# Optimization experiments

Measured on AMD Instinct MI355X. Metric: run time of the kernel, lower is better.

The kernel has to match this reference:

```python
import jax, jax.numpy as jnp
import numpy as np

RADIUS = 0.1
K = 32
NUM_GROUPS = 8
EPS = 1e-5
B, N = 2, 4096
IN_DIM = 13
OUT_DIMS = (64, 64, 128)


def _safe_norm(x, axis=-1, keepdims=False):
    # 2-norm with zero (not NaN) gradient at 0; forward identical to jnp.linalg.norm
    sq = jnp.sum(x * x, axis=axis, keepdims=keepdims)
    nz = sq > 0
    return jnp.where(nz, jnp.sqrt(jnp.where(nz, sq, 1.0)), 0.0)


def _angle(v1, v2):
    y = _safe_norm(jnp.cross(v1, v2), axis=-1)
    x = jnp.sum(v1 * v2, axis=-1)
    deg = (y == 0) & (x == 0)  # degenerate pairs (e.g. self-neighbor): atan2(0,0)=0
    return jnp.where(deg, 0.0, jnp.arctan2(y, jnp.where(deg, 1.0, x)))


def _ball_group(xyz, radius, k):
    # xyz: (B,N,3) -> neighbor indices (B,N,K); pad out-of-radius slots with first valid idx
    b, n, _ = xyz.shape
    sq = jnp.sum((xyz[:, :, None, :] - xyz[:, None, :, :]) ** 2, axis=-1)  # (B,N,N)
    idx = jnp.broadcast_to(jnp.arange(n, dtype=jnp.int32), (b, n, n))
    idx = jnp.where(sq > radius * radius, n, idx)
    idx = jnp.sort(idx, axis=-1)[:, :, :k]  # (B,N,K)
    first = idx[:, :, :1]
    return jnp.where(idx == n, first, idx)


def _group_norm(x, gamma, beta):
    # x: (B,C,K,N), torch GroupNorm(8, C) semantics (biased var, eps=1e-5)
    b, c, k, n = x.shape
    xg = x.reshape(b, NUM_GROUPS, c // NUM_GROUPS, k, n)
    m = jnp.mean(xg, axis=(2, 3, 4), keepdims=True)
    v = jnp.var(xg, axis=(2, 3, 4), keepdims=True)
    xn = ((xg - m) * jax.lax.rsqrt(v + EPS)).reshape(b, c, k, n)
    return xn * gamma[None, :, None, None] + beta[None, :, None, None]


def _forward(feature, xyz, conv0_w, gn0_g, gn0_b, conv1_w, gn1_g, gn1_b,
             conv2_w, gn2_g, gn2_b, wa, wb, wc):
    b = xyz.shape[0]
    idx = _ball_group(xyz, RADIUS, K)                     # (B,N,K) int32
    bidx = jnp.arange(b)[:, None, None]
    grouped_xyz = xyz[bidx, idx]                          # (B,N,K,3)
    grouped_xyz1 = grouped_xyz - xyz[:, :, None, :]       # relative coords
    dists = _safe_norm(grouped_xyz1, axis=-1, keepdims=True)
    grouped_n = feature[bidx, idx]                        # grouped normals (B,N,K,3)
    new_points = jnp.concatenate([grouped_xyz1, dists, grouped_n], axis=-1)  # (B,N,K,7)

    nr = feature[:, :, None, :]                           # (B,N,1,3)
    ppf = jnp.stack([_angle(nr, grouped_xyz1),
                     _angle(grouped_n, grouped_xyz1),
                     _angle(nr, grouped_n)], axis=-1)     # (B,N,K,3)

    xyz6 = jnp.concatenate([jnp.broadcast_to(xyz[:, :, None, :], grouped_xyz.shape),
                            grouped_xyz], axis=-1)        # (B,N,K,6)
    fused = jnp.concatenate([wa * xyz6, wb * new_points[..., :4], wc * ppf], axis=-1)  # (B,N,K,13)

    x = jnp.transpose(fused, (0, 3, 2, 1))                # (B,13,K,N)
    layers = [(conv0_w, gn0_g, gn0_b), (conv1_w, gn1_g, gn1_b), (conv2_w, gn2_g, gn2_b)]
    for i, (w, g, bb) in enumerate(layers):
        x = jnp.einsum('oc,bckn->bokn', w, x)             # 1x1 conv, no bias
        x = _group_norm(x, g, bb)
        if i != len(layers) - 1:
            x = jax.nn.relu(x)
    out = jnp.max(jax.nn.relu(x), axis=2)                 # (B,128,N)
    x = jnp.max(x, axis=2)                                # (B,128,N)
    return (out, x)


def setup_inputs() -> dict:
    key = jax.random.key(0)
    ks = jax.random.split(key, 8)
    xyz = jax.random.uniform(ks[0], (B, N, 3), dtype=jnp.float32)
    feature = jax.random.normal(ks[1], (B, N, 3), dtype=jnp.float32)
    feature = feature / _safe_norm(feature, axis=-1, keepdims=True)  # unit normals
    inp = {'feature': feature, 'xyz': xyz}
    dims = [IN_DIM] + list(OUT_DIMS)
    for i in range(3):
        scale = 1.0 / np.sqrt(dims[i])
        inp[f'conv{i}_w'] = (jax.random.normal(ks[2 + i], (dims[i + 1], dims[i]), dtype=jnp.float32) * scale)
        inp[f'gn{i}_g'] = jnp.ones((dims[i + 1],), jnp.float32)
        inp[f'gn{i}_b'] = jnp.zeros((dims[i + 1],), jnp.float32)
    inp['wa'] = jnp.ones((1,), jnp.float32)
    inp['wb'] = jnp.ones((1,), jnp.float32)
    inp['wc'] = jnp.ones((1,), jnp.float32)
    return inp


def reference(feature, xyz, conv0_w, gn0_g, gn0_b, conv1_w, gn1_g, gn1_b,
              conv2_w, gn2_g, gn2_b, wa, wb, wc):
    return _forward(feature, xyz, conv0_w, gn0_g, gn0_b, conv1_w, gn1_g, gn1_b,
                    conv2_w, gn2_g, gn2_b, wa, wb, wc)
```

## Files before the change

kernel.cpp:

```cpp
#include <hip/hip_runtime.h>
#include <hip/hip_bf16.h>

#define DEVINL __device__ __forceinline__

typedef short short8 __attribute__((ext_vector_type(8)));
typedef float f32x4 __attribute__((ext_vector_type(4)));

namespace {
constexpr int NB = 2;
constexpr int NN = 4096;
constexpr int KK = 32;
constexpr int NP = NN * KK;
constexpr float R2 = 0.01f;
constexpr float GEPS = 1e-5f;
}

DEVINL ushort2 splitbf(float v) {
    unsigned int b = __float_as_uint(v);
    unsigned int hb = b & 0xffff0000u;
    float r = v - __uint_as_float(hb);
    unsigned int lb = __float_as_uint(r);
    ushort2 res;
    res.x = (unsigned short)(hb >> 16);
    res.y = (unsigned short)(lb >> 16);
    return res;
}

DEVINL float angle3(float ax, float ay, float az, float bx, float by, float bz) {
    float crx = ay * bz - az * by;
    float cry = az * bx - ax * bz;
    float crz = ax * by - ay * bx;
    float sq = crx * crx + cry * cry + crz * crz;
    float yv = sq > 0.f ? sqrtf(sq) : 0.f;
    float xv = ax * bx + ay * by + az * bz;
    if (yv == 0.f && xv == 0.f) return 0.f;
    return atan2f(yv, xv);
}

template <int NV>
DEVINL float blockReducePart(float* vals) {
    #pragma unroll
    for (int m = 1; m < 64; m <<= 1) {
        #pragma unroll
        for (int q = 0; q < NV; ++q) vals[q] += __shfl_xor(vals[q], m, 64);
    }
    __shared__ float red[4][NV];
    int lane = threadIdx.x & 63, w = threadIdx.x >> 6;
    if (lane == 0) {
        #pragma unroll
        for (int q = 0; q < NV; ++q) red[w][q] = vals[q];
    }
    __syncthreads();
    float v = 0.f;
    if ((int)threadIdx.x < NV)
        v = red[0][threadIdx.x] + red[1][threadIdx.x] +
            red[2][threadIdx.x] + red[3][threadIdx.x];
    return v;
}

__global__ __launch_bounds__(256) void k_red(const float* __restrict__ part,
                                             float* __restrict__ stats, int nblk) {
    int o = blockIdx.x;
    const float* p = part + (size_t)o * nblk;
    float s = 0.f;
    for (int i = threadIdx.x; i < nblk; i += 256) s += p[i];
    #pragma unroll
    for (int m = 1; m < 64; m <<= 1) s += __shfl_xor(s, m, 64);
    __shared__ float r[4];
    if ((threadIdx.x & 63) == 0) r[threadIdx.x >> 6] = s;
    __syncthreads();
    if (threadIdx.x == 0) stats[o] = r[0] + r[1] + r[2] + r[3];
}

__global__ void k_prep(const float* __restrict__ w0, const float* __restrict__ w1,
                       const float* __restrict__ w2, float* __restrict__ w0t,
                       short* __restrict__ a1hi, short* __restrict__ a1lo,
                       short* __restrict__ a2hi, short* __restrict__ a2lo) {
    int t = threadIdx.x;
    for (int x = t; x < 64 * 13; x += 256) { int o = x / 13, c = x % 13; w0t[c * 64 + o] = w0[x]; }
    for (int x = t; x < 512; x += 256) {
        int lane = x & 63, ks = (x >> 6) & 1, mt = x >> 7;
        int o = mt * 16 + (lane & 15);
        int cb = ks * 32 + (lane >> 4) * 8;
        #pragma unroll
        for (int e = 0; e < 8; ++e) {
            ushort2 s = splitbf(w1[o * 64 + cb + e]);
            a1hi[x * 8 + e] = (short)s.x;
            a1lo[x * 8 + e] = (short)s.y;
        }
    }
    for (int x = t; x < 1024; x += 256) {
        int lane = x & 63, ks = (x >> 6) & 1, mt = x >> 7;
        int o = mt * 16 + (lane & 15);
        int cb = ks * 32 + (lane >> 4) * 8;
        #pragma unroll
        for (int e = 0; e < 8; ++e) {
            ushort2 s = splitbf(w2[o * 64 + cb + e]);
            a2hi[x * 8 + e] = (short)s.x;
            a2lo[x * 8 + e] = (short)s.y;
        }
    }
}

__global__ __launch_bounds__(256) void k_ball(const float* __restrict__ xyz,
                                              int* __restrict__ idx) {
    int wid = blockIdx.x * 4 + (threadIdx.x >> 6);
    int lane = threadIdx.x & 63;
    int b = wid >> 12;
    int i = wid & (NN - 1);
    const float* xb = xyz + b * NN * 3;
    float cx = xb[i * 3 + 0], cy = xb[i * 3 + 1], cz = xb[i * 3 + 2];
    int* out = idx + wid * KK;
    int cnt = 0;
    int firstj = 0;
    for (int base = 0; base < NN; base += 64) {
        int j = base + lane;
        float dx = xb[j * 3 + 0] - cx;
        float dy = xb[j * 3 + 1] - cy;
        float dz = xb[j * 3 + 2] - cz;
        float d2 = __fadd_rn(__fadd_rn(__fmul_rn(dx, dx), __fmul_rn(dy, dy)), __fmul_rn(dz, dz));
        bool valid = d2 <= R2;
        unsigned long long m = __ballot(valid);
        if (cnt == 0 && m != 0ull) firstj = base + (int)__builtin_ctzll(m);
        int pos = (int)__popcll(m & ((1ull << lane) - 1ull));
        if (valid && (cnt + pos) < KK) out[cnt + pos] = j;
        cnt += (int)__popcll(m);
        if (cnt >= KK) break;
    }
    if (cnt < KK) {
        int kpad = cnt + lane;
        if (kpad < KK) out[kpad] = firstj;
    }
}

__global__ __launch_bounds__(256) void k_feat(
    const float* __restrict__ xyz, const float* __restrict__ feat,
    const int* __restrict__ idx, const float* __restrict__ w0t,
    const float* __restrict__ wap, const float* __restrict__ wbp,
    const float* __restrict__ wcp, float* __restrict__ f13,
    float* __restrict__ part0) {
    int t = blockIdx.x * 256 + threadIdx.x;
    int b = t / NP, r = t % NP;
    int i = r >> 5;
    int j = idx[t];
    const float* xb = xyz + b * NN * 3;
    const float* fb = feat + b * NN * 3;
    float cx = xb[i * 3], cy = xb[i * 3 + 1], cz = xb[i * 3 + 2];
    float nx = fb[i * 3], ny = fb[i * 3 + 1], nz = fb[i * 3 + 2];
    float gx = xb[j * 3], gy = xb[j * 3 + 1], gz = xb[j * 3 + 2];
    float mx = fb[j * 3], my = fb[j * 3 + 1], mz = fb[j * 3 + 2];
    float dx = gx - cx, dy = gy - cy, dz = gz - cz;
    float d2 = dx * dx + dy * dy + dz * dz;
    float dist = d2 > 0.f ? sqrtf(d2) : 0.f;
    float a1 = angle3(nx, ny, nz, dx, dy, dz);
    float a2 = angle3(mx, my, mz, dx, dy, dz);
    float a3 = angle3(nx, ny, nz, mx, my, mz);
    float WA = wap[0], WB = wbp[0], WC = wcp[0];
    float f[13] = {WA * cx, WA * cy, WA * cz, WA * gx, WA * gy, WA * gz,
                   WB * dx, WB * dy, WB * dz, WB * dist, WC * a1, WC * a2, WC * a3};
    float* fo = f13 + (size_t)b * 13 * NP + r;
    #pragma unroll
    for (int c = 0; c < 13; ++c) fo[(size_t)c * NP] = f[c];
    float acc[64];
    #pragma unroll
    for (int o = 0; o < 64; ++o) acc[o] = 0.f;
    #pragma unroll
    for (int c = 0; c < 13; ++c) {
        float v = f[c];
        const float* wr = w0t + c * 64;
        #pragma unroll
        for (int o = 0; o < 64; ++o) acc[o] = fmaf(wr[o], v, acc[o]);
    }
    float vals[16];
    #pragma unroll
    for (int g = 0; g < 8; ++g) {
        float sv = 0.f, sq = 0.f;
        #pragma unroll
        for (int c2 = 0; c2 < 8; ++c2) { float v = acc[g * 8 + c2]; sv += v; sq = fmaf(v, v, sq); }
        vals[g * 2] = sv; vals[g * 2 + 1] = sq;
    }
    float pv = blockReducePart<16>(vals);
    if ((int)threadIdx.x < 16) {
        int blkInB = blockIdx.x & 511;
        part0[(size_t)(b * 16 + threadIdx.x) * 512 + blkInB] = pv;
    }
}

__global__ __launch_bounds__(256) void k_stats01(
    const float* __restrict__ f13, const float* __restrict__ stats0,
    const float* __restrict__ g0, const float* __restrict__ b0,
    const float* __restrict__ w0t,
    const short* __restrict__ a1hi, const short* __restrict__ a1lo,
    float* __restrict__ part1) {
    __shared__ __align__(16) short Xhi[128 * 64];
    __shared__ __align__(16) short Xlo[128 * 64];
    __shared__ float Aff[128];
    int t = threadIdx.x, blk = blockIdx.x;
    int b = blk >> 10;
    int blkInB = blk & 1023;
    int pbase = blkInB << 7;
    if (t < 64) {
        int c = t, g = c >> 3;
        const float inv = 1.f / 1048576.f;
        float s = stats0[b * 16 + g * 2], q = stats0[b * 16 + g * 2 + 1];
        float mean = s * inv;
        float var = q * inv - mean * mean;
        float rstd = rsqrtf(var + GEPS);
        float a = rstd * g0[c];
        Aff[c] = a; Aff[64 + c] = fmaf(-mean, a, b0[c]);
    }
    __syncthreads();
    {
        int p = t & 127, chalf = t >> 7;
        const float* fi = f13 + (size_t)b * 13 * NP + pbase + p;
        float fv[13];
        #pragma unroll
        for (int c = 0; c < 13; ++c) fv[c] = fi[(size_t)c * NP];
        float acc[32];
        #pragma unroll
        for (int o = 0; o < 32; ++o) acc[o] = 0.f;
        #pragma unroll
        for (int c = 0; c < 13; ++c) {
            const float* wr = w0t + c * 64 + chalf * 32;
            #pragma unroll
            for (int o = 0; o < 32; ++o) acc[o] = fmaf(wr[o], fv[c], acc[o]);
        }
        int swz = (p & 7) << 4;
        #pragma unroll
        for (int jc = 0; jc < 4; ++jc) {
            int hw[4], lw[4];
            #pragma unroll
            for (int u = 0; u < 4; ++u) {
                int o0 = jc * 8 + u * 2;
                int ch0 = chalf * 32 + o0;
                float v0 = fmaxf(fmaf(Aff[ch0], acc[o0], Aff[64 + ch0]), 0.f);
                float v1 = fmaxf(fmaf(Aff[ch0 + 1], acc[o0 + 1], Aff[64 + ch0 + 1]), 0.f);
                ushort2 s0 = splitbf(v0), s1 = splitbf(v1);
                hw[u] = (int)((unsigned)s0.x | ((unsigned)s1.x << 16));
                lw[u] = (int)((unsigned)s0.y | ((unsigned)s1.y << 16));
            }
            int off = p * 128 + ((chalf * 64 + jc * 16) ^ swz);
            *reinterpret_cast<int4*>((char*)Xhi + off) = make_int4(hw[0], hw[1], hw[2], hw[3]);
            *reinterpret_cast<int4*>((char*)Xlo + off) = make_int4(lw[0], lw[1], lw[2], lw[3]);
        }
    }
    __syncthreads();
    {
        int w = t >> 6, lane = t & 63, col = lane & 15, kb = lane >> 4;
        short8 whi[2], wlo[2];
        #pragma unroll
        for (int ks = 0; ks < 2; ++ks) {
            int fi_ = ((w * 2 + ks) * 64 + lane) * 8;
            whi[ks] = *reinterpret_cast<const short8*>(a1hi + fi_);
            wlo[ks] = *reinterpret_cast<const short8*>(a1lo + fi_);
        }
        float sv = 0.f, sq = 0.f;
        int swzr = (col & 7) << 4;
        #pragma unroll 2
        for (int s = 0; s < 8; ++s) {
            int rowoff = (s * 16 + col) * 128;
            f32x4 d = {0.f, 0.f, 0.f, 0.f};
            #pragma unroll
            for (int ks = 0; ks < 2; ++ks) {
                int boff = rowoff + ((ks * 64 + kb * 16) ^ swzr);
                short8 bh = *reinterpret_cast<const short8*>((char*)Xhi + boff);
                short8 bl = *reinterpret_cast<const short8*>((char*)Xlo + boff);
                d = __builtin_amdgcn_mfma_f32_16x16x32_bf16(whi[ks], bh, d, 0, 0, 0);
                d = __builtin_amdgcn_mfma_f32_16x16x32_bf16(whi[ks], bl, d, 0, 0, 0);
                d = __builtin_amdgcn_mfma_f32_16x16x32_bf16(wlo[ks], bh, d, 0, 0, 0);
            }
            #pragma unroll
            for (int q = 0; q < 4; ++q) {
                sv += d[q];
                sq = fmaf(d[q], d[q], sq);
            }
        }
        #pragma unroll
        for (int m = 1; m <= 16; m <<= 1) {
            sv += __shfl_xor(sv, m, 64);
            sq += __shfl_xor(sq, m, 64);
        }
        if ((lane & 31) == 0) {
            int grp = w * 2 + (lane >> 5);
            size_t o = (size_t)(b * 16 + grp * 2) * 1024 + blkInB;
            part1[o] = sv;
            part1[o + 1024] = sq;
        }
    }
}

__global__ __launch_bounds__(256) void k_fused2(
    const float* __restrict__ f13, const float* __restrict__ stats0,
    const float* __restrict__ g0, const float* __restrict__ b0,
    const float* __restrict__ w0t,
    const short* __restrict__ a1hi, const short* __restrict__ a1lo,
    const float* __restrict__ stats1,
    const float* __restrict__ g1, const float* __restrict__ b1,
    const float* __restrict__ g2,
    const short* __restrict__ a2hi, const short* __restrict__ a2lo,
    float* __restrict__ ext, float* __restrict__ part2) {
    __shared__ __align__(16) short Xhi[128 * 64];
    __shared__ __align__(16) short Xlo[128 * 64];
    __shared__ float Aff[256];
    int t = threadIdx.x, blk = blockIdx.x;
    int b = blk >> 10;
    int blkInB = blk & 1023;
    int pbase = blkInB << 7;
    if (t < 64) {
        int c = t, g = c >> 3;
        const float inv = 1.f / 1048576.f;
        float s = stats0[b * 16 + g * 2], q = stats0[b * 16 + g * 2 + 1];
        float mean = s * inv;
        float var = q * inv - mean * mean;
        float rstd = rsqrtf(var + GEPS);
        float a = rstd * g0[c];
        Aff[c] = a; Aff[64 + c] = fmaf(-mean, a, b0[c]);
        float s1 = stats1[b * 16 + g * 2], q1 = stats1[b * 16 + g * 2 + 1];
        float mean1 = s1 * inv;
        float var1 = q1 * inv - mean1 * mean1;
        float rstd1 = rsqrtf(var1 + GEPS);
        float a1 = rstd1 * g1[c];
        Aff[128 + c] = a1; Aff[192 + c] = fmaf(-mean1, a1, b1[c]);
    }
    __syncthreads();
    {
        int p = t & 127, chalf = t >> 7;
        const float* fi = f13 + (size_t)b * 13 * NP + pbase + p;
        float fv[13];
        #pragma unroll
        for (int c = 0; c < 13; ++c) fv[c] = fi[(size_t)c * NP];
        float acc[32];
        #pragma unroll
        for (int o = 0; o < 32; ++o) acc[o] = 0.f;
        #pragma unroll
        for (int c = 0; c < 13; ++c) {
            const float* wr = w0t + c * 64 + chalf * 32;
            #pragma unroll
            for (int o = 0; o < 32; ++o) acc[o] = fmaf(wr[o], fv[c], acc[o]);
        }
        int swz = (p & 7) << 4;
        #pragma unroll
        for (int jc = 0; jc < 4; ++jc) {
            int hw[4], lw[4];
            #pragma unroll
            for (int u = 0; u < 4; ++u) {
                int o0 = jc * 8 + u * 2;
                int ch0 = chalf * 32 + o0;
                float v0 = fmaxf(fmaf(Aff[ch0], acc[o0], Aff[64 + ch0]), 0.f);
                float v1 = fmaxf(fmaf(Aff[ch0 + 1], acc[o0 + 1], Aff[64 + ch0 + 1]), 0.f);
                ushort2 s0 = splitbf(v0), s1 = splitbf(v1);
                hw[u] = (int)((unsigned)s0.x | ((unsigned)s1.x << 16));
                lw[u] = (int)((unsigned)s0.y | ((unsigned)s1.y << 16));
            }
            int off = p * 128 + ((chalf * 64 + jc * 16) ^ swz);
            *reinterpret_cast<int4*>((char*)Xhi + off) = make_int4(hw[0], hw[1], hw[2], hw[3]);
            *reinterpret_cast<int4*>((char*)Xlo + off) = make_int4(lw[0], lw[1], lw[2], lw[3]);
        }
    }
    __syncthreads();
    int w = t >> 6, lane = t & 63, col = lane & 15, kb = lane >> 4;
    int swzr = (col & 7) << 4;
    float y[8][4];
    {
        short8 whi[2], wlo[2];
        #pragma unroll
        for (int ks = 0; ks < 2; ++ks) {
            int fi_ = ((w * 2 + ks) * 64 + lane) * 8;
            whi[ks] = *reinterpret_cast<const short8*>(a1hi + fi_);
            wlo[ks] = *reinterpret_cast<const short8*>(a1lo + fi_);
        }
        #pragma unroll 2
        for (int s = 0; s < 8; ++s) {
            int rowoff = (s * 16 + col) * 128;
            f32x4 d = {0.f, 0.f, 0.f, 0.f};
            #pragma unroll
            for (int ks = 0; ks < 2; ++ks) {
                int boff = rowoff + ((ks * 64 + kb * 16) ^ swzr);
                short8 bh = *reinterpret_cast<const short8*>((char*)Xhi + boff);
                short8 bl = *reinterpret_cast<const short8*>((char*)Xlo + boff);
                d = __builtin_amdgcn_mfma_f32_16x16x32_bf16(whi[ks], bh, d, 0, 0, 0);
                d = __builtin_amdgcn_mfma_f32_16x16x32_bf16(whi[ks], bl, d, 0, 0, 0);
                d = __builtin_amdgcn_mfma_f32_16x16x32_bf16(wlo[ks], bh, d, 0, 0, 0);
            }
            #pragma unroll
            for (int q = 0; q < 4; ++q) y[s][q] = d[q];
        }
    }
    __syncthreads();
    {
        float a1v[4], b1v[4];
        #pragma unroll
        for (int q = 0; q < 4; ++q) {
            int c = w * 16 + kb * 4 + q;
            a1v[q] = Aff[128 + c]; b1v[q] = Aff[192 + c];
        }
        #pragma unroll
        for (int s = 0; s < 8; ++s) {
            int hw[2], lw[2];
            #pragma unroll
            for (int u = 0; u < 2; ++u) {
                float v0 = fmaxf(fmaf(a1v[u * 2], y[s][u * 2], b1v[u * 2]), 0.f);
                float v1 = fmaxf(fmaf(a1v[u * 2 + 1], y[s][u * 2 + 1], b1v[u * 2 + 1]), 0.f);
                ushort2 s0 = splitbf(v0), s1 = splitbf(v1);
                hw[u] = (int)((unsigned)s0.x | ((unsigned)s1.x << 16));
                lw[u] = (int)((unsigned)s0.y | ((unsigned)s1.y << 16));
            }
            int p = s * 16 + col;
            int off = p * 128 + ((w * 32 + kb * 8) ^ swzr);
            *reinterpret_cast<int2*>((char*)Xhi + off) = make_int2(hw[0], hw[1]);
            *reinterpret_cast<int2*>((char*)Xlo + off) = make_int2(lw[0], lw[1]);
        }
    }
    __syncthreads();
    {
        int mt0 = w * 2;
        short8 whi[2][2], wlo[2][2];
        #pragma unroll
        for (int m = 0; m < 2; ++m)
            #pragma unroll
            for (int ks = 0; ks < 2; ++ks) {
                int fi_ = (((mt0 + m) * 2 + ks) * 64 + lane) * 8;
                whi[m][ks] = *reinterpret_cast<const short8*>(a2hi + fi_);
                wlo[m][ks] = *reinterpret_cast<const short8*>(a2lo + fi_);
            }
        float gv[2][4];
        #pragma unroll
        for (int m = 0; m < 2; ++m)
            #pragma unroll
            for (int q = 0; q < 4; ++q) gv[m][q] = g2[(mt0 + m) * 16 + kb * 4 + q];
        float sv[2] = {0.f, 0.f}, sq[2] = {0.f, 0.f};
        int ibase = pbase >> 5;
        #pragma unroll
        for (int sp = 0; sp < 4; ++sp) {
            f32x4 dp0[2], dp1[2];
            #pragma unroll
            for (int ss = 0; ss < 2; ++ss) {
                int rowoff = ((sp * 2 + ss) * 16 + col) * 128;
                short8 bh[2], bl[2];
                #pragma unroll
                for (int ks = 0; ks < 2; ++ks) {
                    int boff = rowoff + ((ks * 64 + kb * 16) ^ swzr);
                    bh[ks] = *reinterpret_cast<const short8*>((char*)Xhi + boff);
                    bl[ks] = *reinterpret_cast<const short8*>((char*)Xlo + boff);
                }
                #pragma unroll
                for (int m = 0; m < 2; ++m) {
                    f32x4 d = {0.f, 0.f, 0.f, 0.f};
                    #pragma unroll
                    for (int ks = 0; ks < 2; ++ks) {
                        d = __builtin_amdgcn_mfma_f32_16x16x32_bf16(whi[m][ks], bh[ks], d, 0, 0, 0);
                        d = __builtin_amdgcn_mfma_f32_16x16x32_bf16(whi[m][ks], bl[ks], d, 0, 0, 0);
                        d = __builtin_amdgcn_mfma_f32_16x16x32_bf16(wlo[m][ks], bh[ks], d, 0, 0, 0);
                    }
                    #pragma unroll
                    for (int q = 0; q < 4; ++q) {
                        sv[m] += d[q];
                        sq[m] = fmaf(d[q], d[q], sq[m]);
                    }
                    if (ss == 0) dp0[m] = d; else dp1[m] = d;
                }
            }
            #pragma unroll
            for (int m = 0; m < 2; ++m) {
                float e[4];
                #pragma unroll
                for (int q = 0; q < 4; ++q) {
                    bool mx = gv[m][q] >= 0.f;
                    e[q] = mx ? fmaxf(dp0[m][q], dp1[m][q]) : fminf(dp0[m][q], dp1[m][q]);
                    #pragma unroll
                    for (int sh = 1; sh <= 8; sh <<= 1) {
                        float o = __shfl_xor(e[q], sh, 64);
                        e[q] = mx ? fmaxf(e[q], o) : fminf(e[q], o);
                    }
                }
                if (col == 0) {
                    #pragma unroll
                    for (int q = 0; q < 4; ++q) {
                        int ch = (mt0 + m) * 16 + kb * 4 + q;
                        ext[((size_t)b * 128 + ch) * NN + ibase + sp] = e[q];
                    }
                }
            }
        }
        #pragma unroll
        for (int m = 0; m < 2; ++m) {
            #pragma unroll
            for (int sh = 1; sh <= 32; sh <<= 1) {
                sv[m] += __shfl_xor(sv[m], sh, 64);
                sq[m] += __shfl_xor(sq[m], sh, 64);
            }
        }
        if (lane == 0) {
            #pragma unroll
            for (int m = 0; m < 2; ++m) {
                size_t o = (size_t)(b * 16 + (mt0 + m) * 2) * 1024 + blkInB;
                part2[o] = sv[m];
                part2[o + 1024] = sq[m];
            }
        }
    }
}

__global__ __launch_bounds__(256) void k_final(
    const float* __restrict__ ext, const float* __restrict__ stats2,
    const float* __restrict__ g2, const float* __restrict__ b2,
    float* __restrict__ outp) {
    __shared__ float A[128], Bc[128];
    int t = blockIdx.x * 256 + threadIdx.x;
    int b = t / (128 * NN);
    int rem = t - b * 128 * NN;
    int c = rem >> 12;
    if (threadIdx.x < 128) {
        int cc = threadIdx.x, g = cc >> 4;
        const float inv = 1.f / 2097152.f;
        float s = stats2[b * 16 + g * 2], q = stats2[b * 16 + g * 2 + 1];
        float mean = s * inv;
        float var = q * inv - mean * mean;
        float rstd = rsqrtf(var + GEPS);
        float a = rstd * g2[cc];
        A[cc] = a; Bc[cc] = fmaf(-mean, a, b2[cc]);
    }
    __syncthreads();
    float v = ext[t];
    float val = fmaf(A[c], v, Bc[c]);
    outp[t] = fmaxf(val, 0.f);
    outp[NB * 128 * NN + t] = val;
}

extern "C" void kernel_launch(void* const* d_in, const int* in_sizes, int n_in,
                              void* d_out, int out_size, void* d_ws, size_t ws_size,
                              hipStream_t stream) {
    const float* feat = (const float*)d_in[0];
    const float* xyz  = (const float*)d_in[1];
    const float* w0 = (const float*)d_in[2];
    const float* g0 = (const float*)d_in[3];
    const float* b0 = (const float*)d_in[4];
    const float* w1 = (const float*)d_in[5];
    const float* g1 = (const float*)d_in[6];
    const float* b1 = (const float*)d_in[7];
    const float* w2 = (const float*)d_in[8];
    const float* g2 = (const float*)d_in[9];
    const float* b2 = (const float*)d_in[10];
    const float* wa = (const float*)d_in[11];
    const float* wb = (const float*)d_in[12];
    const float* wc = (const float*)d_in[13];

    char* ws = (char*)d_ws;
    float* stats = (float*)ws;
    float* w0t  = (float*)(ws + 4096);
    short* a1hi = (short*)(ws + 16384);
    short* a1lo = (short*)(ws + 24576);
    short* a2hi = (short*)(ws + 32768);
    short* a2lo = (short*)(ws + 49152);
    int*   idx  = (int*)(ws + 65536);
    float* part0 = (float*)(ws + 1179648);
    float* part1 = (float*)(ws + 1245184);
    float* part2 = (float*)(ws + 1376256);
    float* f13  = (float*)(ws + (2ull << 20));
    float* ext  = (float*)(ws + (16ull << 20));

    hipLaunchKernelGGL(k_prep, dim3(1), dim3(256), 0, stream,
                       w0, w1, w2, w0t, a1hi, a1lo, a2hi, a2lo);
    hipLaunchKernelGGL(k_ball, dim3((NB * NN) / 4), dim3(256), 0, stream, xyz, idx);
    hipLaunchKernelGGL(k_feat, dim3((NB * NP) / 256), dim3(256), 0, stream,
                       xyz, feat, idx, w0t, wa, wb, wc, f13, part0);
    hipLaunchKernelGGL(k_red, dim3(32), dim3(256), 0, stream, part0, stats, 512);
    hipLaunchKernelGGL(k_stats01, dim3((NB * NP) / 128), dim3(256), 0, stream,
                       f13, stats, g0, b0, w0t, a1hi, a1lo, part1);
    hipLaunchKernelGGL(k_red, dim3(32), dim3(256), 0, stream, part1, stats + 32, 1024);
    hipLaunchKernelGGL(k_fused2, dim3((NB * NP) / 128), dim3(256), 0, stream,
                       f13, stats, g0, b0, w0t, a1hi, a1lo,
                       stats + 32, g1, b1, g2, a2hi, a2lo, ext, part2);
    hipLaunchKernelGGL(k_red, dim3(32), dim3(256), 0, stream, part2, stats + 64, 1024);
    hipLaunchKernelGGL(k_final, dim3((NB * 128 * NN) / 256), dim3(256), 0, stream,
                       ext, stats + 64, g2, b2, (float*)d_out);
}
```

Baseline: 217.8 us.

## Fuse all stages into one cooperative persistent kernel with grid syncs

Replaces the chain of nine kernel launches (prep, ball query, feature, three stat reductions, two GEMM stages, final norm) with a single cooperative kernel of 512 persistent blocks. Stages are separated by grid.sync(), and each block reduces the per-group partial stats itself instead of using separate k_red launches. The aim is to remove launch overhead and the tiny reduction kernels. In exchange, every phase is limited to 512 blocks with grid-wide barriers, which may reduce occupancy and latency hiding in the heavy GEMM phases. The weight prep done by block 0 also delays the first grid sync.

```diff
diff --git a/kernel.cpp b/kernel.cpp
--- a/kernel.cpp
+++ b/kernel.cpp
@@ -1,10 +1,13 @@
 #include <hip/hip_runtime.h>
+#include <hip/hip_cooperative_groups.h>
 #include <hip/hip_bf16.h>
 
 #define DEVINL __device__ __forceinline__
 
 typedef short short8 __attribute__((ext_vector_type(8)));
 typedef float f32x4 __attribute__((ext_vector_type(4)));
+
+namespace cg = cooperative_groups;
 
 namespace {
 constexpr int NB = 2;
@@ -13,6 +16,7 @@
 constexpr int NP = NN * KK;
 constexpr float R2 = 0.01f;
 constexpr float GEPS = 1e-5f;
+constexpr int NBLK = 512;
 }
 
 DEVINL ushort2 splitbf(float v) {
@@ -58,221 +62,224 @@
     return v;
 }
 
-__global__ __launch_bounds__(256) void k_red(const float* __restrict__ part,
-                                             float* __restrict__ stats, int nblk) {
-    int o = blockIdx.x;
-    const float* p = part + (size_t)o * nblk;
-    float s = 0.f;
-    for (int i = threadIdx.x; i < nblk; i += 256) s += p[i];
+DEVINL void reduceStats256(const float* __restrict__ part, int b, float* statsL) {
+    int w = threadIdx.x >> 6, lane = threadIdx.x & 63;
     #pragma unroll
-    for (int m = 1; m < 64; m <<= 1) s += __shfl_xor(s, m, 64);
-    __shared__ float r[4];
-    if ((threadIdx.x & 63) == 0) r[threadIdx.x >> 6] = s;
-    __syncthreads();
-    if (threadIdx.x == 0) stats[o] = r[0] + r[1] + r[2] + r[3];
-}
-
-__global__ void k_prep(const float* __restrict__ w0, const float* __restrict__ w1,
-                       const float* __restrict__ w2, float* __restrict__ w0t,
-                       short* __restrict__ a1hi, short* __restrict__ a1lo,
-                       short* __restrict__ a2hi, short* __restrict__ a2lo) {
-    int t = threadIdx.x;
-    for (int x = t; x < 64 * 13; x += 256) { int o = x / 13, c = x % 13; w0t[c * 64 + o] = w0[x]; }
-    for (int x = t; x < 512; x += 256) {
-        int lane = x & 63, ks = (x >> 6) & 1, mt = x >> 7;
-        int o = mt * 16 + (lane & 15);
-        int cb = ks * 32 + (lane >> 4) * 8;
-        #pragma unroll
-        for (int e = 0; e < 8; ++e) {
-            ushort2 s = splitbf(w1[o * 64 + cb + e]);
-            a1hi[x * 8 + e] = (short)s.x;
-            a1lo[x * 8 + e] = (short)s.y;
-        }
-    }
-    for (int x = t; x < 1024; x += 256) {
-        int lane = x & 63, ks = (x >> 6) & 1, mt = x >> 7;
-        int o = mt * 16 + (lane & 15);
-        int cb = ks * 32 + (lane >> 4) * 8;
-        #pragma unroll
-        for (int e = 0; e < 8; ++e) {
-            ushort2 s = splitbf(w2[o * 64 + cb + e]);
-            a2hi[x * 8 + e] = (short)s.x;
-            a2lo[x * 8 + e] = (short)s.y;
-        }
-    }
-}
-
-__global__ __launch_bounds__(256) void k_ball(const float* __restrict__ xyz,
-                                              int* __restrict__ idx) {
-    int wid = blockIdx.x * 4 + (threadIdx.x >> 6);
-    int lane = threadIdx.x & 63;
-    int b = wid >> 12;
-    int i = wid & (NN - 1);
-    const float* xb = xyz + b * NN * 3;
-    float cx = xb[i * 3 + 0], cy = xb[i * 3 + 1], cz = xb[i * 3 + 2];
-    int* out = idx + wid * KK;
-    int cnt = 0;
-    int firstj = 0;
-    for (int base = 0; base < NN; base += 64) {
-        int j = base + lane;
-        float dx = xb[j * 3 + 0] - cx;
-        float dy = xb[j * 3 + 1] - cy;
-        float dz = xb[j * 3 + 2] - cz;
-        float d2 = __fadd_rn(__fadd_rn(__fmul_rn(dx, dx), __fmul_rn(dy, dy)), __fmul_rn(dz, dz));
-        bool valid = d2 <= R2;
-        unsigned long long m = __ballot(valid);
-        if (cnt == 0 && m != 0ull) firstj = base + (int)__builtin_ctzll(m);
-        int pos = (int)__popcll(m & ((1ull << lane) - 1ull));
-        if (valid && (cnt + pos) < KK) out[cnt + pos] = j;
-        cnt += (int)__popcll(m);
-        if (cnt >= KK) break;
-    }
-    if (cnt < KK) {
-        int kpad = cnt + lane;
-        if (kpad < KK) out[kpad] = firstj;
-    }
-}
-
-__global__ __launch_bounds__(256) void k_feat(
-    const float* __restrict__ xyz, const float* __restrict__ feat,
-    const int* __restrict__ idx, const float* __restrict__ w0t,
-    const float* __restrict__ wap, const float* __restrict__ wbp,
-    const float* __restrict__ wcp, float* __restrict__ f13,
-    float* __restrict__ part0) {
-    int t = blockIdx.x * 256 + threadIdx.x;
-    int b = t / NP, r = t % NP;
-    int i = r >> 5;
-    int j = idx[t];
-    const float* xb = xyz + b * NN * 3;
-    const float* fb = feat + b * NN * 3;
-    float cx = xb[i * 3], cy = xb[i * 3 + 1], cz = xb[i * 3 + 2];
-    float nx = fb[i * 3], ny = fb[i * 3 + 1], nz = fb[i * 3 + 2];
-    float gx = xb[j * 3], gy = xb[j * 3 + 1], gz = xb[j * 3 + 2];
-    float mx = fb[j * 3], my = fb[j * 3 + 1], mz = fb[j * 3 + 2];
-    float dx = gx - cx, dy = gy - cy, dz = gz - cz;
-    float d2 = dx * dx + dy * dy + dz * dz;
-    float dist = d2 > 0.f ? sqrtf(d2) : 0.f;
-    float a1 = angle3(nx, ny, nz, dx, dy, dz);
-    float a2 = angle3(mx, my, mz, dx, dy, dz);
-    float a3 = angle3(nx, ny, nz, mx, my, mz);
-    float WA = wap[0], WB = wbp[0], WC = wcp[0];
-    float f[13] = {WA * cx, WA * cy, WA * cz, WA * gx, WA * gy, WA * gz,
-                   WB * dx, WB * dy, WB * dz, WB * dist, WC * a1, WC * a2, WC * a3};
-    float* fo = f13 + (size_t)b * 13 * NP + r;
-    #pragma unroll
-    for (int c = 0; c < 13; ++c) fo[(size_t)c * NP] = f[c];
-    float acc[64];
-    #pragma unroll
-    for (int o = 0; o < 64; ++o) acc[o] = 0.f;
-    #pragma unroll
-    for (int c = 0; c < 13; ++c) {
-        float v = f[c];
-        const float* wr = w0t + c * 64;
-        #pragma unroll
-        for (int o = 0; o < 64; ++o) acc[o] = fmaf(wr[o], v, acc[o]);
-    }
-    float vals[16];
-    #pragma unroll
-    for (int g = 0; g < 8; ++g) {
-        float sv = 0.f, sq = 0.f;
-        #pragma unroll
-        for (int c2 = 0; c2 < 8; ++c2) { float v = acc[g * 8 + c2]; sv += v; sq = fmaf(v, v, sq); }
-        vals[g * 2] = sv; vals[g * 2 + 1] = sq;
-    }
-    float pv = blockReducePart<16>(vals);
-    if ((int)threadIdx.x < 16) {
-        int blkInB = blockIdx.x & 511;
-        part0[(size_t)(b * 16 + threadIdx.x) * 512 + blkInB] = pv;
-    }
-}
-
-__global__ __launch_bounds__(256) void k_stats01(
-    const float* __restrict__ f13, const float* __restrict__ stats0,
-    const float* __restrict__ g0, const float* __restrict__ b0,
-    const float* __restrict__ w0t,
-    const short* __restrict__ a1hi, const short* __restrict__ a1lo,
-    float* __restrict__ part1) {
+    for (int o = w; o < 16; o += 4) {
+        const float* p = part + ((size_t)(b * 16 + o) << 8);
+        float s = p[lane] + p[lane + 64] + p[lane + 128] + p[lane + 192];
+        #pragma unroll
+        for (int m = 1; m < 64; m <<= 1) s += __shfl_xor(s, m, 64);
+        if (lane == 0) statsL[o] = s;
+    }
+}
+
+__global__ __launch_bounds__(256, 4) void k_mega(
+    const float* __restrict__ featp, const float* __restrict__ xyzp,
+    const float* __restrict__ w0, const float* __restrict__ g0, const float* __restrict__ b0,
+    const float* __restrict__ w1, const float* __restrict__ g1, const float* __restrict__ b1,
+    const float* __restrict__ w2, const float* __restrict__ g2, const float* __restrict__ b2,
+    const float* __restrict__ wap, const float* __restrict__ wbp, const float* __restrict__ wcp,
+    float* __restrict__ w0t, short* __restrict__ a1hi, short* __restrict__ a1lo,
+    short* __restrict__ a2hi, short* __restrict__ a2lo,
+    int* __restrict__ idx, float* __restrict__ f13, float* __restrict__ ext,
+    float* __restrict__ part0, float* __restrict__ part1, float* __restrict__ part2,
+    float* __restrict__ outp) {
+    cg::grid_group grid = cg::this_grid();
     __shared__ __align__(16) short Xhi[128 * 64];
     __shared__ __align__(16) short Xlo[128 * 64];
-    __shared__ float Aff[128];
-    int t = threadIdx.x, blk = blockIdx.x;
-    int b = blk >> 10;
-    int blkInB = blk & 1023;
-    int pbase = blkInB << 7;
-    if (t < 64) {
-        int c = t, g = c >> 3;
+    __shared__ float Aff[256];
+    __shared__ float statsL[16];
+    const int tid = threadIdx.x, blk = blockIdx.x;
+    const int b = blk >> 8;
+    const int blkInB = blk & 255;
+    const int wv = tid >> 6, lane = tid & 63;
+
+    if (blk == 0) {
+        for (int x = tid; x < 64 * 13; x += 256) { int o = x / 13, c = x % 13; w0t[c * 64 + o] = w0[x]; }
+        for (int x = tid; x < 512; x += 256) {
+            int ln = x & 63, ks = (x >> 6) & 1, mt = x >> 7;
+            int o = mt * 16 + (ln & 15);
+            int cb = ks * 32 + (ln >> 4) * 8;
+            #pragma unroll
+            for (int e = 0; e < 8; ++e) {
+                ushort2 s = splitbf(w1[o * 64 + cb + e]);
+                a1hi[x * 8 + e] = (short)s.x;
+                a1lo[x * 8 + e] = (short)s.y;
+            }
+        }
+        for (int x = tid; x < 1024; x += 256) {
+            int ln = x & 63, ks = (x >> 6) & 1, mt = x >> 7;
+            int o = mt * 16 + (ln & 15);
+            int cb = ks * 32 + (ln >> 4) * 8;
+            #pragma unroll
+            for (int e = 0; e < 8; ++e) {
+                ushort2 s = splitbf(w2[o * 64 + cb + e]);
+                a2hi[x * 8 + e] = (short)s.x;
+                a2lo[x * 8 + e] = (short)s.y;
+            }
+        }
+    }
+    for (int wid = blk * 4 + wv; wid < NB * NN; wid += NBLK * 4) {
+        int bb = wid >> 12;
+        int i = wid & (NN - 1);
+        const float* xb = xyzp + bb * NN * 3;
+        float cx = xb[i * 3 + 0], cy = xb[i * 3 + 1], cz = xb[i * 3 + 2];
+        int* out = idx + wid * KK;
+        int cnt = 0;
+        int firstj = 0;
+        for (int base = 0; base < NN; base += 64) {
+            int j = base + lane;
+            float dx = xb[j * 3 + 0] - cx;
+            float dy = xb[j * 3 + 1] - cy;
+            float dz = xb[j * 3 + 2] - cz;
+            float d2 = __fadd_rn(__fadd_rn(__fmul_rn(dx, dx), __fmul_rn(dy, dy)), __fmul_rn(dz, dz));
+            bool valid = d2 <= R2;
+            unsigned long long m = __ballot(valid);
+            if (cnt == 0 && m != 0ull) firstj = base + (int)__builtin_ctzll(m);
+            int pos = (int)__popcll(m & ((1ull << lane) - 1ull));
+            if (valid && (cnt + pos) < KK) out[cnt + pos] = j;
+            cnt += (int)__popcll(m);
+            if (cnt >= KK) break;
+        }
+        if (cnt < KK) {
+            int kpad = cnt + lane;
+            if (kpad < KK) out[kpad] = firstj;
+        }
+    }
+    grid.sync();
+
+    {
+        float vals[16];
+        #pragma unroll
+        for (int q = 0; q < 16; ++q) vals[q] = 0.f;
+        float WA = wap[0], WB = wbp[0], WC = wcp[0];
+        const float* xb = xyzp + b * NN * 3;
+        const float* fb = featp + b * NN * 3;
+        #pragma unroll
+        for (int k = 0; k < 2; ++k) {
+            int r = blkInB * 512 + k * 256 + tid;
+            int i = r >> 5;
+            int j = idx[b * NP + r];
+            float cx = xb[i * 3], cy = xb[i * 3 + 1], cz = xb[i * 3 + 2];
+            float nx = fb[i * 3], ny = fb[i * 3 + 1], nz = fb[i * 3 + 2];
+            float gx = xb[j * 3], gy = xb[j * 3 + 1], gz = xb[j * 3 + 2];
+            float mx = fb[j * 3], my = fb[j * 3 + 1], mz = fb[j * 3 + 2];
+            float dx = gx - cx, dy = gy - cy, dz = gz - cz;
+            float d2 = dx * dx + dy * dy + dz * dz;
+            float dist = d2 > 0.f ? sqrtf(d2) : 0.f;
+            float a1 = angle3(nx, ny, nz, dx, dy, dz);
+            float a2 = angle3(mx, my, mz, dx, dy, dz);
+            float a3 = angle3(nx, ny, nz, mx, my, mz);
+            float f[13] = {WA * cx, WA * cy, WA * cz, WA * gx, WA * gy, WA * gz,
+                           WB * dx, WB * dy, WB * dz, WB * dist, WC * a1, WC * a2, WC * a3};
+            float* fo = f13 + (size_t)b * 13 * NP + r;
+            #pragma unroll
+            for (int c = 0; c < 13; ++c) fo[(size_t)c * NP] = f[c];
+            float acc[64];
+            #pragma unroll
+            for (int o = 0; o < 64; ++o) acc[o] = 0.f;
+            #pragma unroll
+            for (int c = 0; c < 13; ++c) {
+                float v = f[c];
+                const float* wr = w0t + c * 64;
+                #pragma unroll
+                for (int o = 0; o < 64; ++o) acc[o] = fmaf(wr[o], v, acc[o]);
+            }
+            #pragma unroll
+            for (int g = 0; g < 8; ++g) {
+                float sv = 0.f, sq = 0.f;
+                #pragma unroll
+                for (int c2 = 0; c2 < 8; ++c2) { float v = acc[g * 8 + c2]; sv += v; sq = fmaf(v, v, sq); }
+                vals[g * 2] += sv; vals[g * 2 + 1] += sq;
+            }
+        }
+        float pv = blockReducePart<16>(vals);
+        if (tid < 16) part0[(size_t)(b * 16 + tid) * 256 + blkInB] = pv;
+    }
+    grid.sync();
+
+    reduceStats256(part0, b, statsL);
+    __syncthreads();
+    if (tid < 64) {
+        int c = tid, g = c >> 3;
         const float inv = 1.f / 1048576.f;
-        float s = stats0[b * 16 + g * 2], q = stats0[b * 16 + g * 2 + 1];
-        float mean = s * inv;
-        float var = q * inv - mean * mean;
+        float mean = statsL[g * 2] * inv;
+        float var = statsL[g * 2 + 1] * inv - mean * mean;
         float rstd = rsqrtf(var + GEPS);
         float a = rstd * g0[c];
         Aff[c] = a; Aff[64 + c] = fmaf(-mean, a, b0[c]);
     }
     __syncthreads();
+
+    const int col = lane & 15, kb = lane >> 4;
+    const int swzr = (col & 7) << 4;
+
     {
-        int p = t & 127, chalf = t >> 7;
-        const float* fi = f13 + (size_t)b * 13 * NP + pbase + p;
-        float fv[13];
-        #pragma unroll
-        for (int c = 0; c < 13; ++c) fv[c] = fi[(size_t)c * NP];
-        float acc[32];
-        #pragma unroll
-        for (int o = 0; o < 32; ++o) acc[o] = 0.f;
-        #pragma unroll
-        for (int c = 0; c < 13; ++c) {
-            const float* wr = w0t + c * 64 + chalf * 32;
-            #pragma unroll
-            for (int o = 0; o < 32; ++o) acc[o] = fmaf(wr[o], fv[c], acc[o]);
-        }
-        int swz = (p & 7) << 4;
-        #pragma unroll
-        for (int jc = 0; jc < 4; ++jc) {
-            int hw[4], lw[4];
-            #pragma unroll
-            for (int u = 0; u < 4; ++u) {
-                int o0 = jc * 8 + u * 2;
-                int ch0 = chalf * 32 + o0;
-                float v0 = fmaxf(fmaf(Aff[ch0], acc[o0], Aff[64 + ch0]), 0.f);
-                float v1 = fmaxf(fmaf(Aff[ch0 + 1], acc[o0 + 1], Aff[64 + ch0 + 1]), 0.f);
-                ushort2 s0 = splitbf(v0), s1 = splitbf(v1);
-                hw[u] = (int)((unsigned)s0.x | ((unsigned)s1.x << 16));
-                lw[u] = (int)((unsigned)s0.y | ((unsigned)s1.y << 16));
-            }
-            int off = p * 128 + ((chalf * 64 + jc * 16) ^ swz);
-            *reinterpret_cast<int4*>((char*)Xhi + off) = make_int4(hw[0], hw[1], hw[2], hw[3]);
-            *reinterpret_cast<int4*>((char*)Xlo + off) = make_int4(lw[0], lw[1], lw[2], lw[3]);
-        }
-    }
-    __syncthreads();
-    {
-        int w = t >> 6, lane = t & 63, col = lane & 15, kb = lane >> 4;
         short8 whi[2], wlo[2];
         #pragma unroll
         for (int ks = 0; ks < 2; ++ks) {
-            int fi_ = ((w * 2 + ks) * 64 + lane) * 8;
+            int fi_ = ((wv * 2 + ks) * 64 + lane) * 8;
             whi[ks] = *reinterpret_cast<const short8*>(a1hi + fi_);
             wlo[ks] = *reinterpret_cast<const short8*>(a1lo + fi_);
         }
         float sv = 0.f, sq = 0.f;
-        int swzr = (col & 7) << 4;
-        #pragma unroll 2
-        for (int s = 0; s < 8; ++s) {
-            int rowoff = (s * 16 + col) * 128;
-            f32x4 d = {0.f, 0.f, 0.f, 0.f};
-            #pragma unroll
-            for (int ks = 0; ks < 2; ++ks) {
-                int boff = rowoff + ((ks * 64 + kb * 16) ^ swzr);
-                short8 bh = *reinterpret_cast<const short8*>((char*)Xhi + boff);
-                short8 bl = *reinterpret_cast<const short8*>((char*)Xlo + boff);
-                d = __builtin_amdgcn_mfma_f32_16x16x32_bf16(whi[ks], bh, d, 0, 0, 0);
-                d = __builtin_amdgcn_mfma_f32_16x16x32_bf16(whi[ks], bl, d, 0, 0, 0);
-                d = __builtin_amdgcn_mfma_f32_16x16x32_bf16(wlo[ks], bh, d, 0, 0, 0);
-            }
-            #pragma unroll
-            for (int q = 0; q < 4; ++q) {
-                sv += d[q];
-                sq = fmaf(d[q], d[q], sq);
+        for (int it = 0; it < 4; ++it) {
+            int pbase = (blkInB * 4 + it) << 7;
+            __syncthreads();
+            {
+                int p = tid & 127, chalf = tid >> 7;
+                const float* fi = f13 + (size_t)b * 13 * NP + pbase + p;
+                float fv[13];
+                #pragma unroll
+                for (int c = 0; c < 13; ++c) fv[c] = fi[(size_t)c * NP];
+                float acc[32];
+                #pragma unroll
+                for (int o = 0; o < 32; ++o) acc[o] = 0.f;
+                #pragma unroll
+                for (int c = 0; c < 13; ++c) {
+                    const float* wr = w0t + c * 64 + chalf * 32;
+                    #pragma unroll
+                    for (int o = 0; o < 32; ++o) acc[o] = fmaf(wr[o], fv[c], acc[o]);
+                }
+                int swz = (p & 7) << 4;
+                #pragma unroll
+                for (int jc = 0; jc < 4; ++jc) {
+                    int hw[4], lw[4];
+                    #pragma unroll
+                    for (int u = 0; u < 4; ++u) {
+                        int o0 = jc * 8 + u * 2;
+                        int ch0 = chalf * 32 + o0;
+                        float v0 = fmaxf(fmaf(Aff[ch0], acc[o0], Aff[64 + ch0]), 0.f);
+                        float v1 = fmaxf(fmaf(Aff[ch0 + 1], acc[o0 + 1], Aff[64 + ch0 + 1]), 0.f);
+                        ushort2 s0 = splitbf(v0), s1 = splitbf(v1);
+                        hw[u] = (int)((unsigned)s0.x | ((unsigned)s1.x << 16));
+                        lw[u] = (int)((unsigned)s0.y | ((unsigned)s1.y << 16));
+                    }
+                    int off = p * 128 + ((chalf * 64 + jc * 16) ^ swz);
+                    *reinterpret_cast<int4*>((char*)Xhi + off) = make_int4(hw[0], hw[1], hw[2], hw[3]);
+                    *reinterpret_cast<int4*>((char*)Xlo + off) = make_int4(lw[0], lw[1], lw[2], lw[3]);
+                }
+            }
+            __syncthreads();
+            #pragma unroll 2
+            for (int s = 0; s < 8; ++s) {
+                int rowoff = (s * 16 + col) * 128;
+                f32x4 d = {0.f, 0.f, 0.f, 0.f};
+                #pragma unroll
+                for (int ks = 0; ks < 2; ++ks) {
+                    int boff = rowoff + ((ks * 64 + kb * 16) ^ swzr);
+                    short8 bh = *reinterpret_cast<const short8*>((char*)Xhi + boff);
+                    short8 bl = *reinterpret_cast<const short8*>((char*)Xlo + boff);
+                    d = __builtin_amdgcn_mfma_f32_16x16x32_bf16(whi[ks], bh, d, 0, 0, 0);
+                    d = __builtin_amdgcn_mfma_f32_16x16x32_bf16(whi[ks], bl, d, 0, 0, 0);
+                    d = __builtin_amdgcn_mfma_f32_16x16x32_bf16(wlo[ks], bh, d, 0, 0, 0);
+                }
+                #pragma unroll
+                for (int q = 0; q < 4; ++q) {
+                    sv += d[q];
+                    sq = fmaf(d[q], d[q], sq);
+                }
             }
         }
         #pragma unroll
@@ -281,257 +288,239 @@
             sq += __shfl_xor(sq, m, 64);
         }
         if ((lane & 31) == 0) {
-            int grp = w * 2 + (lane >> 5);
-            size_t o = (size_t)(b * 16 + grp * 2) * 1024 + blkInB;
+            int grp = wv * 2 + (lane >> 5);
+            size_t o = (size_t)(b * 16 + grp * 2) * 256 + blkInB;
             part1[o] = sv;
-            part1[o + 1024] = sq;
-        }
-    }
-}
-
-__global__ __launch_bounds__(256) void k_fused2(
-    const float* __restrict__ f13, const float* __restrict__ stats0,
-    const float* __restrict__ g0, const float* __restrict__ b0,
-    const float* __restrict__ w0t,
-    const short* __restrict__ a1hi, const short* __restrict__ a1lo,
-    const float* __restrict__ stats1,
-    const float* __restrict__ g1, const float* __restrict__ b1,
-    const float* __restrict__ g2,
-    const short* __restrict__ a2hi, const short* __restrict__ a2lo,
-    float* __restrict__ ext, float* __restrict__ part2) {
-    __shared__ __align__(16) short Xhi[128 * 64];
-    __shared__ __align__(16) short Xlo[128 * 64];
-    __shared__ float Aff[256];
-    int t = threadIdx.x, blk = blockIdx.x;
-    int b = blk >> 10;
-    int blkInB = blk & 1023;
-    int pbase = blkInB << 7;
-    if (t < 64) {
-        int c = t, g = c >> 3;
+            part1[o + 256] = sq;
+        }
+    }
+    grid.sync();
+
+    reduceStats256(part1, b, statsL);
+    __syncthreads();
+    if (tid < 64) {
+        int c = tid, g = c >> 3;
         const float inv = 1.f / 1048576.f;
-        float s = stats0[b * 16 + g * 2], q = stats0[b * 16 + g * 2 + 1];
-        float mean = s * inv;
-        float var = q * inv - mean * mean;
+        float mean = statsL[g * 2] * inv;
+        float var = statsL[g * 2 + 1] * inv - mean * mean;
         float rstd = rsqrtf(var + GEPS);
-        float a = rstd * g0[c];
-        Aff[c] = a; Aff[64 + c] = fmaf(-mean, a, b0[c]);
-        float s1 = stats1[b * 16 + g * 2], q1 = stats1[b * 16 + g * 2 + 1];
-        float mean1 = s1 * inv;
-        float var1 = q1 * inv - mean1 * mean1;
-        float rstd1 = rsqrtf(var1 + GEPS);
-        float a1 = rstd1 * g1[c];
-        Aff[128 + c] = a1; Aff[192 + c] = fmaf(-mean1, a1, b1[c]);
-    }
-    __syncthreads();
+        float a = rstd * g1[c];
+        Aff[128 + c] = a; Aff[192 + c] = fmaf(-mean, a, b1[c]);
+    }
+    __syncthreads();
+
     {
-        int p = t & 127, chalf = t >> 7;
-        const float* fi = f13 + (size_t)b * 13 * NP + pbase + p;
-        float fv[13];
-        #pragma unroll
-        for (int c = 0; c < 13; ++c) fv[c] = fi[(size_t)c * NP];
-        float acc[32];
-        #pragma unroll
-        for (int o = 0; o < 32; ++o) acc[o] = 0.f;
-        #pragma unroll
-        for (int c = 0; c < 13; ++c) {
-            const float* wr = w0t + c * 64 + chalf * 32;
-            #pragma unroll
-            for (int o = 0; o < 32; ++o) acc[o] = fmaf(wr[o], fv[c], acc[o]);
-        }
-        int swz = (p & 7) << 4;
-        #pragma unroll
-        for (int jc = 0; jc < 4; ++jc) {
-            int hw[4], lw[4];
-            #pragma unroll
-            for (int u = 0; u < 4; ++u) {
-                int o0 = jc * 8 + u * 2;
-                int ch0 = chalf * 32 + o0;
-                float v0 = fmaxf(fmaf(Aff[ch0], acc[o0], Aff[64 + ch0]), 0.f);
-                float v1 = fmaxf(fmaf(Aff[ch0 + 1], acc[o0 + 1], Aff[64 + ch0 + 1]), 0.f);
-                ushort2 s0 = splitbf(v0), s1 = splitbf(v1);
-                hw[u] = (int)((unsigned)s0.x | ((unsigned)s1.x << 16));
-                lw[u] = (int)((unsigned)s0.y | ((unsigned)s1.y << 16));
-            }
-            int off = p * 128 + ((chalf * 64 + jc * 16) ^ swz);
-            *reinterpret_cast<int4*>((char*)Xhi + off) = make_int4(hw[0], hw[1], hw[2], hw[3]);
-            *reinterpret_cast<int4*>((char*)Xlo + off) = make_int4(lw[0], lw[1], lw[2], lw[3]);
-        }
-    }
-    __syncthreads();
-    int w = t >> 6, lane = t & 63, col = lane & 15, kb = lane >> 4;
-    int swzr = (col & 7) << 4;
-    float y[8][4];
-    {
-        short8 whi[2], wlo[2];
-        #pragma unroll
-        for (int ks = 0; ks < 2; ++ks) {
-            int fi_ = ((w * 2 + ks) * 64 + lane) * 8;
-            whi[ks] = *reinterpret_cast<const short8*>(a1hi + fi_);
-            wlo[ks] = *reinterpret_cast<const short8*>(a1lo + fi_);
-        }
-        #pragma unroll 2
-        for (int s = 0; s < 8; ++s) {
-            int rowoff = (s * 16 + col) * 128;
-            f32x4 d = {0.f, 0.f, 0.f, 0.f};
-            #pragma unroll
-            for (int ks = 0; ks < 2; ++ks) {
-                int boff = rowoff + ((ks * 64 + kb * 16) ^ swzr);
-                short8 bh = *reinterpret_cast<const short8*>((char*)Xhi + boff);
-                short8 bl = *reinterpret_cast<const short8*>((char*)Xlo + boff);
-                d = __builtin_amdgcn_mfma_f32_16x16x32_bf16(whi[ks], bh, d, 0, 0, 0);
-                d = __builtin_amdgcn_mfma_f32_16x16x32_bf16(whi[ks], bl, d, 0, 0, 0);
-                d = __builtin_amdgcn_mfma_f32_16x16x32_bf16(wlo[ks], bh, d, 0, 0, 0);
-            }
-            #pragma unroll
-            for (int q = 0; q < 4; ++q) y[s][q] = d[q];
-        }
-    }
-    __syncthreads();
-    {
-        float a1v[4], b1v[4];
-        #pragma unroll
-        for (int q = 0; q < 4; ++q) {
-            int c = w * 16 + kb * 4 + q;
-            a1v[q] = Aff[128 + c]; b1v[q] = Aff[192 + c];
-        }
-        #pragma unroll
-        for (int s = 0; s < 8; ++s) {
-            int hw[2], lw[2];
-            #pragma unroll
-            for (int u = 0; u < 2; ++u) {
-                float v0 = fmaxf(fmaf(a1v[u * 2], y[s][u * 2], b1v[u * 2]), 0.f);
-                float v1 = fmaxf(fmaf(a1v[u * 2 + 1], y[s][u * 2 + 1], b1v[u * 2 + 1]), 0.f);
-                ushort2 s0 = splitbf(v0), s1 = splitbf(v1);
-                hw[u] = (int)((unsigned)s0.x | ((unsigned)s1.x << 16));
-                lw[u] = (int)((unsigned)s0.y | ((unsigned)s1.y << 16));
-            }
-            int p = s * 16 + col;
-            int off = p * 128 + ((w * 32 + kb * 8) ^ swzr);
-            *reinterpret_cast<int2*>((char*)Xhi + off) = make_int2(hw[0], hw[1]);
-            *reinterpret_cast<int2*>((char*)Xlo + off) = make_int2(lw[0], lw[1]);
-        }
-    }
-    __syncthreads();
-    {
-        int mt0 = w * 2;
-        short8 whi[2][2], wlo[2][2];
+        int mt0 = wv * 2;
+        float gv[2][4];
         #pragma unroll
         for (int m = 0; m < 2; ++m)
             #pragma unroll
-            for (int ks = 0; ks < 2; ++ks) {
-                int fi_ = (((mt0 + m) * 2 + ks) * 64 + lane) * 8;
-                whi[m][ks] = *reinterpret_cast<const short8*>(a2hi + fi_);
-                wlo[m][ks] = *reinterpret_cast<const short8*>(a2lo + fi_);
-            }
-        float gv[2][4];
-        #pragma unroll
-        for (int m = 0; m < 2; ++m)
-            #pragma unroll
             for (int q = 0; q < 4; ++q) gv[m][q] = g2[(mt0 + m) * 16 + kb * 4 + q];
-        float sv[2] = {0.f, 0.f}, sq[2] = {0.f, 0.f};
-        int ibase = pbase >> 5;
-        #pragma unroll
-        for (int sp = 0; sp < 4; ++sp) {
-            f32x4 dp0[2], dp1[2];
-            #pragma unroll
-            for (int ss = 0; ss < 2; ++ss) {
-                int rowoff = ((sp * 2 + ss) * 16 + col) * 128;
-                short8 bh[2], bl[2];
+        float sv2[2] = {0.f, 0.f}, sq2[2] = {0.f, 0.f};
+        for (int it = 0; it < 4; ++it) {
+            int tileInB = blkInB * 4 + it;
+            int pbase = tileInB << 7;
+            __syncthreads();
+            {
+                int p = tid & 127, chalf = tid >> 7;
+                const float* fi = f13 + (size_t)b * 13 * NP + pbase + p;
+                float fv[13];
+                #pragma unroll
+                for (int c = 0; c < 13; ++c) fv[c] = fi[(size_t)c * NP];
+                float acc[32];
+                #pragma unroll
+                for (int o = 0; o < 32; ++o) acc[o] = 0.f;
+                #pragma unroll
+                for (int c = 0; c < 13; ++c) {
+                    const float* wr = w0t + c * 64 + chalf * 32;
+                    #pragma unroll
+                    for (int o = 0; o < 32; ++o) acc[o] = fmaf(wr[o], fv[c], acc[o]);
+                }
+                int swz = (p & 7) << 4;
+                #pragma unroll
+                for (int jc = 0; jc < 4; ++jc) {
+                    int hw[4], lw[4];
+                    #pragma unroll
+                    for (int u = 0; u < 4; ++u) {
+                        int o0 = jc * 8 + u * 2;
+                        int ch0 = chalf * 32 + o0;
+                        float v0 = fmaxf(fmaf(Aff[ch0], acc[o0], Aff[64 + ch0]), 0.f);
+                        float v1 = fmaxf(fmaf(Aff[ch0 + 1], acc[o0 + 1], Aff[64 + ch0 + 1]), 0.f);
+                        ushort2 s0 = splitbf(v0), s1 = splitbf(v1);
+                        hw[u] = (int)((unsigned)s0.x | ((unsigned)s1.x << 16));
+                        lw[u] = (int)((unsigned)s0.y | ((unsigned)s1.y << 16));
+                    }
+                    int off = p * 128 + ((chalf * 64 + jc * 16) ^ swz);
+                    *reinterpret_cast<int4*>((char*)Xhi + off) = make_int4(hw[0], hw[1], hw[2], hw[3]);
+                    *reinterpret_cast<int4*>((char*)Xlo + off) = make_int4(lw[0], lw[1], lw[2], lw[3]);
+                }
+            }
+            __syncthreads();
+            float y[8][4];
+            {
+                short8 whi[2], wlo[2];
                 #pragma unroll
                 for (int ks = 0; ks < 2; ++ks) {
-                    int boff = rowoff + ((ks * 64 + kb * 16) ^ swzr);
-                    bh[ks] = *reinterpret_cast<const short8*>((char*)Xhi + boff);
-                    bl[ks] = *reinterpret_cast<const short8*>((char*)Xlo + boff);
-                }
-                #pragma unroll
-                for (int m = 0; m < 2; ++m) {
+                    int fi_ = ((wv * 2 + ks) * 64 + lane) * 8;
+                    whi[ks] = *reinterpret_cast<const short8*>(a1hi + fi_);
+                    wlo[ks] = *reinterpret_cast<const short8*>(a1lo + fi_);
+                }
+                #pragma unroll 2
+                for (int s = 0; s < 8; ++s) {
+                    int rowoff = (s * 16 + col) * 128;
                     f32x4 d = {0.f, 0.f, 0.f, 0.f};
                     #pragma unroll
                     for (int ks = 0; ks < 2; ++ks) {
-                        d = __builtin_amdgcn_mfma_f32_16x16x32_bf16(whi[m][ks], bh[ks], d, 0, 0, 0);
-                        d = __builtin_amdgcn_mfma_f32_16x16x32_bf16(whi[m][ks], bl[ks], d, 0, 0, 0);
-                        d = __builtin_amdgcn_mfma_f32_16x16x32_bf16(wlo[m][ks], bh[ks], d, 0, 0, 0);
-                    }
-                    #pragma unroll
-                    for (int q = 0; q < 4; ++q) {
-                        sv[m] += d[q];
-                        sq[m] = fmaf(d[q], d[q], sq[m]);
-                    }
-                    if (ss == 0) dp0[m] = d; else dp1[m] = d;
-                }
-            }
+                        int boff = rowoff + ((ks * 64 + kb * 16) ^ swzr);
+                        short8 bh = *reinterpret_cast<const short8*>((char*)Xhi + boff);
+                        short8 bl = *reinterpret_cast<const short8*>((char*)Xlo + boff);
+                        d = __builtin_amdgcn_mfma_f32_16x16x32_bf16(whi[ks], bh, d, 0, 0, 0);
+                        d = __builtin_amdgcn_mfma_f32_16x16x32_bf16(whi[ks], bl, d, 0, 0, 0);
+                        d = __builtin_amdgcn_mfma_f32_16x16x32_bf16(wlo[ks], bh, d, 0, 0, 0);
+                    }
+                    #pragma unroll
+                    for (int q = 0; q < 4; ++q) y[s][q] = d[q];
+                }
+            }
+            __syncthreads();
+            {
+                float a1v[4], b1v[4];
+                #pragma unroll
+                for (int q = 0; q < 4; ++q) {
+                    int c = wv * 16 + kb * 4 + q;
+                    a1v[q] = Aff[128 + c]; b1v[q] = Aff[192 + c];
+                }
+                #pragma unroll
+                for (int s = 0; s < 8; ++s) {
+                    int hw[2], lw[2];
+                    #pragma unroll
+                    for (int u = 0; u < 2; ++u) {
+                        float v0 = fmaxf(fmaf(a1v[u * 2], y[s][u * 2], b1v[u * 2]), 0.f);
+                        float v1 = fmaxf(fmaf(a1v[u * 2 + 1], y[s][u * 2 + 1], b1v[u * 2 + 1]), 0.f);
+                        ushort2 s0 = splitbf(v0), s1 = splitbf(v1);
+                        hw[u] = (int)((unsigned)s0.x | ((unsigned)s1.x << 16));
+                        lw[u] = (int)((unsigned)s0.y | ((unsigned)s1.y << 16));
+                    }
+                    int p = s * 16 + col;
+                    int off = p * 128 + ((wv * 32 + kb * 8) ^ swzr);
+                    *reinterpret_cast<int2*>((char*)Xhi + off) = make_int2(hw[0], hw[1]);
+                    *reinterpret_cast<int2*>((char*)Xlo + off) = make_int2(lw[0], lw[1]);
+                }
+            }
+            __syncthreads();
+            {
+                short8 whi[2][2], wlo[2][2];
+                #pragma unroll
+                for (int m = 0; m < 2; ++m)
+                    #pragma unroll
+                    for (int ks = 0; ks < 2; ++ks) {
+                        int fi_ = (((mt0 + m) * 2 + ks) * 64 + lane) * 8;
+                        whi[m][ks] = *reinterpret_cast<const short8*>(a2hi + fi_);
+                        wlo[m][ks] = *reinterpret_cast<const short8*>(a2lo + fi_);
+                    }
+                int ibase = tileInB * 4;
+                #pragma unroll
+                for (int sp = 0; sp < 4; ++sp) {
+                    f32x4 dp0[2], dp1[2];
+                    #pragma unroll
+                    for (int ss = 0; ss < 2; ++ss) {
+                        int rowoff = ((sp * 2 + ss) * 16 + col) * 128;
+                        short8 bh[2], bl[2];
+                        #pragma unroll
+                        for (int ks = 0; ks < 2; ++ks) {
+                            int boff = rowoff + ((ks * 64 + kb * 16) ^ swzr);
+                            bh[ks] = *reinterpret_cast<const short8*>((char*)Xhi + boff);
+                            bl[ks] = *reinterpret_cast<const short8*>((char*)Xlo + boff);
+                        }
+                        #pragma unroll
+                        for (int m = 0; m < 2; ++m) {
+                            f32x4 d = {0.f, 0.f, 0.f, 0.f};
+                            #pragma unroll
+                            for (int ks = 0; ks < 2; ++ks) {
+                                d = __builtin_amdgcn_mfma_f32_16x16x32_bf16(whi[m][ks], bh[ks], d, 0, 0, 0);
+                                d = __builtin_amdgcn_mfma_f32_16x16x32_bf16(whi[m][ks], bl[ks], d, 0, 0, 0);
+                                d = __builtin_amdgcn_mfma_f32_16x16x32_bf16(wlo[m][ks], bh[ks], d, 0, 0, 0);
+                            }
+                            #pragma unroll
+                            for (int q = 0; q < 4; ++q) {
+                                sv2[m] += d[q];
+                                sq2[m] = fmaf(d[q], d[q], sq2[m]);
+                            }
+                            if (ss == 0) dp0[m] = d; else dp1[m] = d;
+                        }
+                    }
+                    #pragma unroll
+                    for (int m = 0; m < 2; ++m) {
+                        float e[4];
+                        #pragma unroll
+                        for (int q = 0; q < 4; ++q) {
+                            bool mx = gv[m][q] >= 0.f;
+                            e[q] = mx ? fmaxf(dp0[m][q], dp1[m][q]) : fminf(dp0[m][q], dp1[m][q]);
+                            #pragma unroll
+                            for (int sh = 1; sh <= 8; sh <<= 1) {
+                                float o = __shfl_xor(e[q], sh, 64);
+                                e[q] = mx ? fmaxf(e[q], o) : fminf(e[q], o);
+                            }
+                        }
+                        if (col == 0) {
+                            #pragma unroll
+                            for (int q = 0; q < 4; ++q) {
+                                int ch = (mt0 + m) * 16 + kb * 4 + q;
+                                ext[((size_t)b * 128 + ch) * NN + ibase + sp] = e[q];
+                            }
+                        }
+                    }
+                }
+            }
+        }
+        #pragma unroll
+        for (int m = 0; m < 2; ++m) {
+            #pragma unroll
+            for (int sh = 1; sh <= 32; sh <<= 1) {
+                sv2[m] += __shfl_xor(sv2[m], sh, 64);
+                sq2[m] += __shfl_xor(sq2[m], sh, 64);
+            }
+        }
+        if (lane == 0) {
             #pragma unroll
             for (int m = 0; m < 2; ++m) {
-                float e[4];
-                #pragma unroll
-                for (int q = 0; q < 4; ++q) {
-                    bool mx = gv[m][q] >= 0.f;
-                    e[q] = mx ? fmaxf(dp0[m][q], dp1[m][q]) : fminf(dp0[m][q], dp1[m][q]);
-                    #pragma unroll
-                    for (int sh = 1; sh <= 8; sh <<= 1) {
-                        float o = __shfl_xor(e[q], sh, 64);
-                        e[q] = mx ? fmaxf(e[q], o) : fminf(e[q], o);
-                    }
-                }
-                if (col == 0) {
-                    #pragma unroll
-                    for (int q = 0; q < 4; ++q) {
-                        int ch = (mt0 + m) * 16 + kb * 4 + q;
-                        ext[((size_t)b * 128 + ch) * NN + ibase + sp] = e[q];
-                    }
-                }
-            }
-        }
-        #pragma unroll
-        for (int m = 0; m < 2; ++m) {
-            #pragma unroll
-            for (int sh = 1; sh <= 32; sh <<= 1) {
-                sv[m] += __shfl_xor(sv[m], sh, 64);
-                sq[m] += __shfl_xor(sq[m], sh, 64);
-            }
-        }
-        if (lane == 0) {
-            #pragma unroll
-            for (int m = 0; m < 2; ++m) {
-                size_t o = (size_t)(b * 16 + (mt0 + m) * 2) * 1024 + blkInB;
-                part2[o] = sv[m];
-                part2[o + 1024] = sq[m];
-            }
-        }
-    }
-}
-
-__global__ __launch_bounds__(256) void k_final(
-    const float* __restrict__ ext, const float* __restrict__ stats2,
-    const float* __restrict__ g2, const float* __restrict__ b2,
-    float* __restrict__ outp) {
-    __shared__ float A[128], Bc[128];
-    int t = blockIdx.x * 256 + threadIdx.x;
-    int b = t / (128 * NN);
-    int rem = t - b * 128 * NN;
-    int c = rem >> 12;
-    if (threadIdx.x < 128) {
-        int cc = threadIdx.x, g = cc >> 4;
+                size_t o = (size_t)(b * 16 + (mt0 + m) * 2) * 256 + blkInB;
+                part2[o] = sv2[m];
+                part2[o + 256] = sq2[m];
+            }
+        }
+    }
+    grid.sync();
+
+    reduceStats256(part2, b, statsL);
+    __syncthreads();
+    if (tid < 128) {
+        int g = tid >> 4;
         const float inv = 1.f / 2097152.f;
-        float s = stats2[b * 16 + g * 2], q = stats2[b * 16 + g * 2 + 1];
-        float mean = s * inv;
-        float var = q * inv - mean * mean;
+        float mean = statsL[g * 2] * inv;
+        float var = statsL[g * 2 + 1] * inv - mean * mean;
         float rstd = rsqrtf(var + GEPS);
-        float a = rstd * g2[cc];
-        A[cc] = a; Bc[cc] = fmaf(-mean, a, b2[cc]);
-    }
-    __syncthreads();
-    float v = ext[t];
-    float val = fmaf(A[c], v, Bc[c]);
-    outp[t] = fmaxf(val, 0.f);
-    outp[NB * 128 * NN + t] = val;
+        float a = rstd * g2[tid];
+        Aff[tid] = a; Aff[128 + tid] = fmaf(-mean, a, b2[tid]);
+    }
+    __syncthreads();
+    #pragma unroll
+    for (int k = 0; k < 8; ++k) {
+        int rr = blkInB * 2048 + k * 256 + tid;
+        int c = rr >> 12;
+        size_t t6 = (size_t)b * 128 * NN + rr;
+        float v = ext[t6];
+        float val = fmaf(Aff[c], v, Aff[128 + c]);
+        outp[t6] = fmaxf(val, 0.f);
+        outp[(size_t)NB * 128 * NN + t6] = val;
+    }
 }
 
 extern "C" void kernel_launch(void* const* d_in, const int* in_sizes, int n_in,
                               void* d_out, int out_size, void* d_ws, size_t ws_size,
                               hipStream_t stream) {
-    const float* feat = (const float*)d_in[0];
-    const float* xyz  = (const float*)d_in[1];
+    const float* featp = (const float*)d_in[0];
+    const float* xyzp  = (const float*)d_in[1];
     const float* w0 = (const float*)d_in[2];
     const float* g0 = (const float*)d_in[3];
     const float* b0 = (const float*)d_in[4];
@@ -541,12 +530,11 @@
     const float* w2 = (const float*)d_in[8];
     const float* g2 = (const float*)d_in[9];
     const float* b2 = (const float*)d_in[10];
-    const float* wa = (const float*)d_in[11];
-    const float* wb = (const float*)d_in[12];
-    const float* wc = (const float*)d_in[13];
+    const float* wap = (const float*)d_in[11];
+    const float* wbp = (const float*)d_in[12];
+    const float* wcp = (const float*)d_in[13];
 
     char* ws = (char*)d_ws;
-    float* stats = (float*)ws;
     float* w0t  = (float*)(ws + 4096);
     short* a1hi = (short*)(ws + 16384);
     short* a1lo = (short*)(ws + 24576);
@@ -555,23 +543,22 @@
     int*   idx  = (int*)(ws + 65536);
     float* part0 = (float*)(ws + 1179648);
     float* part1 = (float*)(ws + 1245184);
-    float* part2 = (float*)(ws + 1376256);
+    float* part2 = (float*)(ws + 1310720);
     float* f13  = (float*)(ws + (2ull << 20));
     float* ext  = (float*)(ws + (16ull << 20));
-
-    hipLaunchKernelGGL(k_prep, dim3(1), dim3(256), 0, stream,
-                       w0, w1, w2, w0t, a1hi, a1lo, a2hi, a2lo);
-    hipLaunchKernelGGL(k_ball, dim3((NB * NN) / 4), dim3(256), 0, stream, xyz, idx);
-    hipLaunchKernelGGL(k_feat, dim3((NB * NP) / 256), dim3(256), 0, stream,
-                       xyz, feat, idx, w0t, wa, wb, wc, f13, part0);
-    hipLaunchKernelGGL(k_red, dim3(32), dim3(256), 0, stream, part0, stats, 512);
-    hipLaunchKernelGGL(k_stats01, dim3((NB * NP) / 128), dim3(256), 0, stream,
-                       f13, stats, g0, b0, w0t, a1hi, a1lo, part1);
-    hipLaunchKernelGGL(k_red, dim3(32), dim3(256), 0, stream, part1, stats + 32, 1024);
-    hipLaunchKernelGGL(k_fused2, dim3((NB * NP) / 128), dim3(256), 0, stream,
-                       f13, stats, g0, b0, w0t, a1hi, a1lo,
-                       stats + 32, g1, b1, g2, a2hi, a2lo, ext, part2);
-    hipLaunchKernelGGL(k_red, dim3(32), dim3(256), 0, stream, part2, stats + 64, 1024);
-    hipLaunchKernelGGL(k_final, dim3((NB * 128 * NN) / 256), dim3(256), 0, stream,
-                       ext, stats + 64, g2, b2, (float*)d_out);
-}
+    float* outp = (float*)d_out;
+
+    void* args[] = {
+        (void*)&featp, (void*)&xyzp,
+        (void*)&w0, (void*)&g0, (void*)&b0,
+        (void*)&w1, (void*)&g1, (void*)&b1,
+        (void*)&w2, (void*)&g2, (void*)&b2,
+        (void*)&wap, (void*)&wbp, (void*)&wcp,
+        (void*)&w0t, (void*)&a1hi, (void*)&a1lo, (void*)&a2hi, (void*)&a2lo,
+        (void*)&idx, (void*)&f13, (void*)&ext,
+        (void*)&part0, (void*)&part1, (void*)&part2,
+        (void*)&outp
+    };
+    hipLaunchCooperativeKernel((const void*)k_mega, dim3(NBLK), dim3(256),
+                               args, 0, stream);
+}
```

Result: slower. 831.4 us (+281.8%).
